# Kernel tuning notes

Hardware: AMD Instinct MI355X
Metric: run time of the kernel (lower is better)

## Reference

```python
import jax, jax.numpy as jnp
import numpy as np

B, R, C, E, H = 2, 16, 512, 1024, 16
D = E // H  # head_dim = 64


def setup_inputs() -> dict:
    key = jax.random.key(0)
    ks = jax.random.split(key, 9)
    s = 1.0 / np.sqrt(E)
    return {
        "x": jax.random.normal(ks[0], (B, R, C, E), dtype=jnp.float32),
        "wq": jax.random.uniform(ks[1], (E, E), jnp.float32, -s, s),
        "bq": jax.random.uniform(ks[2], (E,), jnp.float32, -s, s),
        "wk": jax.random.uniform(ks[3], (E, E), jnp.float32, -s, s),
        "bk": jax.random.uniform(ks[4], (E,), jnp.float32, -s, s),
        "wv": jax.random.uniform(ks[5], (E, E), jnp.float32, -s, s),
        "bv": jax.random.uniform(ks[6], (E,), jnp.float32, -s, s),
        "wo": jax.random.uniform(ks[7], (E, E), jnp.float32, -s, s),
        "bo": jax.random.uniform(ks[8], (E,), jnp.float32, -s, s),
    }


def reference(x, wq, bq, wk, bk, wv, bv, wo, bo):
    b, r, c, e = x.shape
    # projections: [b,r,c,e] -> [b,r,h,c,d]
    def split_heads(t):
        return t.reshape(b, r, c, H, D).transpose(0, 1, 3, 2, 4)
    q = split_heads(x @ wq + bq)
    k = split_heads(x @ wk + bk)
    v = split_heads(x @ wv + bv)
    scale = 1.0 / jnp.sqrt(jnp.asarray(D, x.dtype))
    logits = jnp.einsum('brhqd,brhkd->brhqk', q, k) * scale
    probs = jax.nn.softmax(logits, axis=-1)
    ctx = jnp.einsum('brhqk,brhkd->brhqd', probs, v)
    ctx = ctx.transpose(0, 1, 3, 2, 4).reshape(b, r, c, e)
    return ctx @ wo + bo
```

## Files before the change

kernel.cpp:

```cpp
#include <hip/hip_runtime.h>
#include <hip/hip_bf16.h>
#include <hip/hip_fp16.h>
#include <math.h>

typedef _Float16 half8 __attribute__((ext_vector_type(8)));
typedef __attribute__((ext_vector_type(4))) float floatx4;

constexpr int Bc = 2, Rc = 16, Cc = 512, Ec = 1024, Hc = 16, Dc = 64;
#define QSCALE 0.180336880111120425f

__device__ inline void gl_lds16(const void* g, void* l) {
  __builtin_amdgcn_global_load_lds(
      (const __attribute__((address_space(1))) void*)g,
      (__attribute__((address_space(3))) void*)l, 16, 0, 0);
}
__device__ inline unsigned short f2h(float f) {
  __half h = __float2half_rn(f);
  return *(unsigned short*)&h;
}
__device__ inline unsigned int pack_h2(float lo, float hi) {
  __half2 p = __float22half2_rn(make_float2(lo, hi));
  return *(unsigned int*)&p;
}

__global__ __launch_bounds__(256) void cvt_x(const float* __restrict__ x,
                                             unsigned short* __restrict__ xh) {
  const size_t base = ((size_t)blockIdx.x * 256 + threadIdx.x) * 8;
  float4 a = *(const float4*)(x + base);
  float4 b = *(const float4*)(x + base + 4);
  uint4 o;
  o.x = pack_h2(a.x, a.y);
  o.y = pack_h2(a.z, a.w);
  o.z = pack_h2(b.x, b.y);
  o.w = pack_h2(b.z, b.w);
  *(uint4*)(xh + base) = o;
}

__global__ __launch_bounds__(256) void wprep(
    const float* __restrict__ w0, const float* __restrict__ w1,
    const float* __restrict__ w2, const float* __restrict__ w3,
    unsigned short* __restrict__ t0, unsigned short* __restrict__ t1,
    unsigned short* __restrict__ t2, unsigned short* __restrict__ t3) {
  __shared__ float tile[64][65];
  const int z = blockIdx.z;
  const float* W = (z == 0) ? w0 : (z == 1) ? w1 : (z == 2) ? w2 : w3;
  unsigned short* T = (z == 0) ? t0 : (z == 1) ? t1 : (z == 2) ? t2 : t3;
  const int tid = threadIdx.x;
  const int bk = blockIdx.x * 64, bn = blockIdx.y * 64;
#pragma unroll
  for (int p = 0; p < 16; ++p) {
    int idx = p * 256 + tid;
    int lk = idx >> 6, lnn = idx & 63;
    tile[lnn][lk] = W[(size_t)(bk + lk) * 1024 + bn + lnn];
  }
  __syncthreads();
  const int lane = tid & 63, sub = tid >> 6;
  const int lr = lane & 15, quad = lane >> 4;
#pragma unroll
  for (int tl = 0; tl < 2; ++tl) {
    float v[8];
#pragma unroll
    for (int jj = 0; jj < 8; ++jj)
      v[jj] = tile[sub * 16 + lr][tl * 32 + quad * 8 + jj];
    uint4 o;
    o.x = pack_h2(v[0], v[1]);
    o.y = pack_h2(v[2], v[3]);
    o.z = pack_h2(v[4], v[5]);
    o.w = pack_h2(v[6], v[7]);
    const size_t n16 = (size_t)(bn >> 4) + sub;
    const size_t tt = (size_t)(bk >> 5) + tl;
    *(uint4*)(T + ((n16 * 32 + tt) * 64 + lane) * 8) = o;
  }
}

#define WAIT_VM(N)                                                            \
  {                                                                           \
    __builtin_amdgcn_sched_barrier(0);                                        \
    asm volatile("s_waitcnt vmcnt(" #N ")" ::: "memory");                     \
    __builtin_amdgcn_sched_barrier(0);                                        \
  }

#define STG_A(SBUF, KT)                                                       \
  {                                                                           \
    _Pragma("unroll") for (int l_ = 0; l_ < 2; ++l_) {                        \
      const int r0_ = l_ * 128 + w * 16;                                      \
      gl_lds16(Ab + (size_t)r0_ * 1024 + glan + (size_t)(KT) * 32,            \
               As + (SBUF) * 8192 + r0_ * 32);                                \
    }                                                                         \
  }

#define BLOAD(FB, KT)                                                         \
  _Pragma("unroll") for (int j_ = 0; j_ < 4; ++j_) FB[j_] =                   \
      *(const half8*)(Bf + bqoff + (size_t)j_ * 16384 + (size_t)(KT) * 512);

#define DSRA(NBUF, FA)                                                        \
  _Pragma("unroll") for (int i_ = 0; i_ < 8; ++i_) FA[i_] =                   \
      *(const half8*)&As[(NBUF) * 8192 + (wm + i_ * 16 + lr) * 32 + swq];

#define MFMA32(FA, FB)                                                        \
  _Pragma("unroll") for (int i_ = 0; i_ < 8; ++i_)                            \
      _Pragma("unroll") for (int j_ = 0; j_ < 4; ++j_) acc[i_][j_] =          \
          __builtin_amdgcn_mfma_f32_16x16x32_f16(FA[i_], FB[j_],              \
                                                 acc[i_][j_], 0, 0, 0);

#define TSTEP(NBUF, SBUF, KSTG, KBLD, FA, FB, NFA, NFB, STGE, BLDE, DSRE,     \
              VMN, BARE)                                                      \
  {                                                                           \
    if (STGE) STG_A(SBUF, KSTG);                                              \
    if (BLDE) BLOAD(NFB, KBLD);                                               \
    if (DSRE) DSRA(NBUF, NFA);                                                \
    WAIT_VM(VMN);                                                             \
    __builtin_amdgcn_s_setprio(1);                                            \
    MFMA32(FA, FB);                                                           \
    __builtin_amdgcn_s_setprio(0);                                            \
    if (BARE) {                                                               \
      __builtin_amdgcn_s_barrier();                                           \
      __builtin_amdgcn_sched_barrier(0);                                      \
    }                                                                         \
  }

template <int MODE>
__global__ __launch_bounds__(512, 2) void gemm256(
    const unsigned short* __restrict__ gA, const unsigned short* __restrict__ gB,
    const float* __restrict__ bq, const float* __restrict__ bk,
    const float* __restrict__ bv, unsigned short* __restrict__ qout,
    unsigned short* __restrict__ kout, unsigned short* __restrict__ vout,
    float* __restrict__ fout, const float* __restrict__ bo) {
  __shared__ unsigned short As[4 * 8192];
  const int tid = threadIdx.x;
  const int w = tid >> 6, ln = tid & 63;
  const int lr = ln & 15, quad = ln >> 4;
  const int wm = (w >> 2) * 128, wn = (w & 3) * 64;
  int bm, bn;
  if (MODE == 0) {
    const int swz = (blockIdx.x & 7) * 96 + (blockIdx.x >> 3);
    bm = (swz / 12) * 256;
    bn = (swz % 12) * 256;
  } else {
    const int swz = (blockIdx.x & 7) * 32 + (blockIdx.x >> 3);
    bm = (swz >> 2) * 256;
    bn = (swz & 3) * 256;
  }
  const unsigned short* Ab = gA + (size_t)bm * 1024;
  const unsigned short* Bf = gB;
  const size_t bqoff =
      (size_t)((bn >> 4) + (w & 3) * 4) * 16384 + (size_t)ln * 8;
  const int glan = (ln >> 2) * 1024 + (((ln & 3) ^ ((ln >> 3) & 3)) << 3);
  const int swq = ((quad ^ ((lr >> 1) & 3)) << 3);

  floatx4 acc[8][4];
#pragma unroll
  for (int i = 0; i < 8; ++i)
#pragma unroll
    for (int j = 0; j < 4; ++j) acc[i][j] = (floatx4)(0.f);
  half8 fa0[8], fa1[8], fb0[4], fb1[4];

  STG_A(0, 0);
  STG_A(1, 1);
  STG_A(2, 2);
  BLOAD(fb0, 0);
  WAIT_VM(6);
  __builtin_amdgcn_s_barrier();
  __builtin_amdgcn_sched_barrier(0);
  DSRA(0, fa0);

  for (int tt = 0; tt < 7; ++tt) {
    const int k4 = tt * 4;
    TSTEP(1, 3, k4 + 3, k4 + 1, fa0, fb0, fa1, fb1, 1, 1, 1, 6, 1);
    TSTEP(2, 0, k4 + 4, k4 + 2, fa1, fb1, fa0, fb0, 1, 1, 1, 6, 1);
    TSTEP(3, 1, k4 + 5, k4 + 3, fa0, fb0, fa1, fb1, 1, 1, 1, 6, 1);
    TSTEP(0, 2, k4 + 6, k4 + 4, fa1, fb1, fa0, fb0, 1, 1, 1, 6, 1);
  }
  TSTEP(1, 3, 31, 29, fa0, fb0, fa1, fb1, 1, 1, 1, 6, 1);
  TSTEP(2, 0, 0, 30, fa1, fb1, fa0, fb0, 0, 1, 1, 4, 1);
  TSTEP(3, 0, 0, 31, fa0, fb0, fa1, fb1, 0, 1, 1, 4, 1);
  TSTEP(0, 0, 0, 0, fa1, fb1, fa0, fb0, 0, 0, 0, 0, 0);

  const int q4 = quad * 4;
  const bool odd = ln & 1;
  if constexpr (MODE == 0) {
    const int z = bn >> 10;
    const float* bias = (z == 0) ? bq : (z == 1) ? bk : bv;
    const int czb = (bn & 1023) + wn;
#pragma unroll
    for (int i = 0; i < 8; ++i) {
#pragma unroll
      for (int j = 0; j < 4; ++j) {
        const int colz = czb + j * 16 + lr;
        float v[4];
#pragma unroll
        for (int r = 0; r < 4; ++r) v[r] = acc[i][j][r] + bias[colz];
        const int m0 = bm + wm + i * 16 + q4;
        const int h = colz >> 6, d = colz & 63;
        const int brr = m0 >> 9, c0 = m0 & 511;
        const size_t hb = ((size_t)brr * 16 + h) * 32768;
        if (z == 2) {
          uint2 o;
          o.x = pack_h2(v[0], v[1]);
          o.y = pack_h2(v[2], v[3]);
          *(uint2*)(vout + hb + (size_t)d * 512 + c0) = o;
        } else {
          unsigned short* outp = (z == 0) ? qout : kout;
          if (z == 0) {
#pragma unroll
            for (int r = 0; r < 4; ++r) v[r] *= QSCALE;
          }
#pragma unroll
          for (int rp = 0; rp < 2; ++rp) {
            float a = v[2 * rp], b = v[2 * rp + 1];
            float ax = __shfl_xor(a, 1), bx = __shfl_xor(b, 1);
            unsigned int u = odd ? pack_h2(bx, b) : pack_h2(a, ax);
            const int c = c0 + 2 * rp + (odd ? 1 : 0);
            const int dd = d & ~1;
            *(unsigned int*)(outp + hb + (size_t)c * 64 + dd) = u;
          }
        }
      }
    }
  } else {
#pragma unroll
    for (int i = 0; i < 8; ++i)
#pragma unroll
      for (int j = 0; j < 4; ++j) {
        const int col = bn + wn + j * 16 + lr;
#pragma unroll
        for (int r = 0; r < 4; ++r) {
          const int m = bm + wm + i * 16 + q4 + r;
          fout[(size_t)m * 1024 + col] = acc[i][j][r] + bo[col];
        }
      }
  }
}

__global__ __launch_bounds__(256, 4) void attn_mfma(
    const unsigned short* __restrict__ Qh, const unsigned short* __restrict__ Kb,
    const unsigned short* __restrict__ Vt, unsigned short* __restrict__ Ctx) {
  __shared__ unsigned short Ks[64 * 64];
  __shared__ unsigned short Vs[64 * 64];
  __shared__ unsigned short Ps[128][72];

  const int t = threadIdx.x;
  const int w = t >> 6, ln = t & 63;
  const int lane15 = ln & 15, quad = ln >> 4;
  const bool odd = ln & 1;
  const int bh = (blockIdx.x & 7) * 64 + (blockIdx.x >> 5);
  const int qb = ((blockIdx.x >> 3) & 3) * 128;

  half8 qf[2][2];
  {
    const size_t qbase =
        ((size_t)bh * 512 + qb + w * 32 + lane15) * 64 + quad * 8;
#pragma unroll
    for (int i = 0; i < 2; ++i)
#pragma unroll
      for (int c = 0; c < 2; ++c)
        qf[i][c] = *(const half8*)(Qh + qbase + (size_t)i * 16 * 64 + c * 32);
  }

  floatx4 oacc[2][4];
#pragma unroll
  for (int i = 0; i < 2; ++i)
#pragma unroll
    for (int dj = 0; dj < 4; ++dj) oacc[i][dj] = (floatx4)(0.f);
  float lsum[2][4];
#pragma unroll
  for (int i = 0; i < 2; ++i)
#pragma unroll
    for (int r = 0; r < 4; ++r) lsum[i][r] = 0.f;

  const unsigned short* kgb = Kb + (size_t)bh * 32768;
  const unsigned short* vgb = Vt + (size_t)bh * 32768;

  uint4 k0r, k1r, v0r, v1r;
#define LDK(P, KT)                                                            \
  (*(const uint4*)((const char*)kgb + (size_t)(KT) * 128 +                    \
                   (size_t)((P) * 256 + t) * 16))
#define LDV(P, KT)                                                            \
  (*(const uint4*)((const char*)vgb + (size_t)(KT) * 2 +                      \
                   (size_t)(((P) * 256 + t) >> 3) * 1024 +                    \
                   (((P) * 256 + t) & 7) * 16))
#define AT_LOAD(KT)                                                           \
  { k0r = LDK(0, KT); k1r = LDK(1, KT); v0r = LDV(0, KT); v1r = LDV(1, KT); }
#define STK(P, R)                                                             \
  {                                                                           \
    const int s_ = (P) * 256 + t, kr_ = s_ >> 3, kc_ = s_ & 7;                \
    *(uint4*)((char*)Ks + kr_ * 128 + ((kc_ ^ (kr_ & 7)) << 4)) = R;          \
  }
#define STV(P, R)                                                             \
  {                                                                           \
    const int s_ = (P) * 256 + t, vr_ = s_ >> 3, vc_ = s_ & 7;                \
    *(uint4*)((char*)Vs + vr_ * 128 + ((vc_ ^ (vr_ & 7)) << 4)) = R;          \
  }
#define AT_WRITE                                                              \
  { STK(0, k0r); STK(1, k1r); STV(0, v0r); STV(1, v1r); }

  AT_LOAD(0);
  AT_WRITE;

#pragma unroll
  for (int ktt = 0; ktt < 8; ++ktt) {
    __syncthreads();

    floatx4 sacc[2][4];
#pragma unroll
    for (int i = 0; i < 2; ++i)
#pragma unroll
      for (int j = 0; j < 4; ++j) sacc[i][j] = (floatx4)(0.f);
    __builtin_amdgcn_s_setprio(1);
#pragma unroll
    for (int j = 0; j < 4; ++j) {
      const int krow = j * 16 + lane15;
      const unsigned short* kr = Ks + krow * 64;
      half8 kf0 = *(const half8*)(kr + ((quad ^ (krow & 7)) << 3));
      half8 kf1 = *(const half8*)(kr + (((4 + quad) ^ (krow & 7)) << 3));
#pragma unroll
      for (int i = 0; i < 2; ++i) {
        sacc[i][j] = __builtin_amdgcn_mfma_f32_16x16x32_f16(qf[i][0], kf0,
                                                            sacc[i][j], 0, 0, 0);
        sacc[i][j] = __builtin_amdgcn_mfma_f32_16x16x32_f16(qf[i][1], kf1,
                                                            sacc[i][j], 0, 0, 0);
      }
    }
    __builtin_amdgcn_s_setprio(0);

#pragma unroll
    for (int i = 0; i < 2; ++i) {
#pragma unroll
      for (int rp = 0; rp < 2; ++rp) {
        const int rA = rp * 2, rB = rA + 1;
        const int row = w * 32 + i * 16 + quad * 4 + rA + (odd ? 1 : 0);
        unsigned short* prow = &Ps[row][lane15 & ~1];
#pragma unroll
        for (int j = 0; j < 4; ++j) {
          const float pA = exp2f(sacc[i][j][rA]);
          const float pB = exp2f(sacc[i][j][rB]);
          lsum[i][rA] += pA;
          lsum[i][rB] += pB;
          const float an = __shfl_xor(pA, 1);
          const float bn = __shfl_xor(pB, 1);
          const float lo = odd ? bn : pA;
          const float hi = odd ? pB : an;
          *(unsigned int*)(prow + j * 16) = pack_h2(lo, hi);
        }
      }
    }

    if (ktt < 7) {
      AT_LOAD((ktt + 1) * 64);
      __builtin_amdgcn_sched_barrier(0);
    }

    __builtin_amdgcn_s_setprio(1);
#pragma unroll
    for (int kc = 0; kc < 2; ++kc) {
      half8 pa0 = *(const half8*)&Ps[w * 32 + lane15][kc * 32 + quad * 8];
      half8 pa1 = *(const half8*)&Ps[w * 32 + 16 + lane15][kc * 32 + quad * 8];
#pragma unroll
      for (int dj = 0; dj < 4; ++dj) {
        const int drow = dj * 16 + lane15;
        half8 vf = *(const half8*)(
            Vs + drow * 64 + (((kc * 4 + quad) ^ (drow & 7)) << 3));
        oacc[0][dj] = __builtin_amdgcn_mfma_f32_16x16x32_f16(pa0, vf,
                                                             oacc[0][dj], 0, 0, 0);
        oacc[1][dj] = __builtin_amdgcn_mfma_f32_16x16x32_f16(pa1, vf,
                                                             oacc[1][dj], 0, 0, 0);
      }
    }
    __builtin_amdgcn_s_setprio(0);

    __syncthreads();
    if (ktt < 7) AT_WRITE;
  }

  float invl[2][4];
#pragma unroll
  for (int i = 0; i < 2; ++i)
#pragma unroll
    for (int r = 0; r < 4; ++r) {
      float ls = lsum[i][r];
#pragma unroll
      for (int off = 1; off < 16; off <<= 1) ls += __shfl_xor(ls, off);
      invl[i][r] = 1.f / ls;
    }
  const int br = bh >> 4, h = bh & 15;
  const size_t mbase = (size_t)br * 512 + qb + w * 32;
#pragma unroll
  for (int i = 0; i < 2; ++i)
#pragma unroll
    for (int dj = 0; dj < 4; ++dj) {
      const int e = h * 64 + dj * 16 + lane15;
      const int ee = e & ~1;
#pragma unroll
      for (int rp = 0; rp < 2; ++rp) {
        const int rA = 2 * rp, rB = rA + 1;
        float a = oacc[i][dj][rA] * invl[i][rA];
        float b = oacc[i][dj][rB] * invl[i][rB];
        float ax = __shfl_xor(a, 1), bx = __shfl_xor(b, 1);
        unsigned int u = odd ? pack_h2(bx, b) : pack_h2(a, ax);
        const size_t m = mbase + i * 16 + quad * 4 + rA + (odd ? 1 : 0);
        *(unsigned int*)(Ctx + m * 1024 + ee) = u;
      }
    }
}

extern "C" void kernel_launch(void* const* d_in, const int* in_sizes, int n_in,
                              void* d_out, int out_size, void* d_ws,
                              size_t ws_size, hipStream_t stream) {
  const float* x = (const float*)d_in[0];
  const float* wq = (const float*)d_in[1];
  const float* bq = (const float*)d_in[2];
  const float* wk = (const float*)d_in[3];
  const float* bk = (const float*)d_in[4];
  const float* wv = (const float*)d_in[5];
  const float* bv = (const float*)d_in[6];
  const float* wo = (const float*)d_in[7];
  const float* bo = (const float*)d_in[8];
  float* out = (float*)d_out;

  char* w = (char*)d_ws;
  const size_t MiB = 1ull << 20;
  unsigned short* qbuf = (unsigned short*)(w + 0 * MiB);
  unsigned short* kbuf = (unsigned short*)(w + 32 * MiB);
  unsigned short* vtb = (unsigned short*)(w + 64 * MiB);
  unsigned short* xh = (unsigned short*)(w + 96 * MiB);
  unsigned short* ctx = (unsigned short*)(w + 128 * MiB);
  unsigned short* wqh = (unsigned short*)(w + 160 * MiB);
  unsigned short* wkh = (unsigned short*)(w + 162 * MiB);
  unsigned short* wvh = (unsigned short*)(w + 164 * MiB);
  unsigned short* woh = (unsigned short*)(w + 166 * MiB);

  cvt_x<<<8192, 256, 0, stream>>>(x, xh);
  wprep<<<dim3(16, 16, 4), 256, 0, stream>>>(wq, wk, wv, wo, wqh, wkh, wvh,
                                             woh);

  gemm256<0><<<768, 512, 0, stream>>>(xh, wqh, bq, bk, bv, qbuf, kbuf, vtb,
                                      nullptr, nullptr);

  attn_mfma<<<2048, 256, 0, stream>>>(qbuf, kbuf, vtb, ctx);

  gemm256<1><<<256, 512, 0, stream>>>(ctx, woh, nullptr, nullptr, nullptr,
                                      nullptr, nullptr, nullptr, out, bo);
}
```

Before: 345.0 us.

## Double-buffer K/V via direct global-to-LDS loads and keep P in registers

The attention kernel now stages K and V tiles with global_load_lds straight into double-buffered LDS slots, prefetching the next tile while the current one is computed. This drops one of the two barriers per iteration. It also swaps the MFMA operand order so scores come out transposed, which lets P stay in registers and be reshuffled with ds_bpermute instead of round-tripping through an LDS P buffer. Row sums become per-lane column sums reduced with two shuffles, and output stores become 8-byte vector writes. The risks are the correctness of the swizzle and permutation indexing, plus the extra bpermute traffic.

```diff
diff --git a/kernel.cpp b/kernel.cpp
--- a/kernel.cpp
+++ b/kernel.cpp
@@ -235,14 +235,12 @@
 __global__ __launch_bounds__(256, 4) void attn_mfma(
     const unsigned short* __restrict__ Qh, const unsigned short* __restrict__ Kb,
     const unsigned short* __restrict__ Vt, unsigned short* __restrict__ Ctx) {
-  __shared__ unsigned short Ks[64 * 64];
-  __shared__ unsigned short Vs[64 * 64];
-  __shared__ unsigned short Ps[128][72];
+  __shared__ unsigned short Kd[2 * 4096];
+  __shared__ unsigned short Vd[2 * 4096];
 
   const int t = threadIdx.x;
   const int w = t >> 6, ln = t & 63;
   const int lane15 = ln & 15, quad = ln >> 4;
-  const bool odd = ln & 1;
   const int bh = (blockIdx.x & 7) * 64 + (blockIdx.x >> 5);
   const int qb = ((blockIdx.x >> 3) & 3) * 128;
 
@@ -257,49 +255,41 @@
         qf[i][c] = *(const half8*)(Qh + qbase + (size_t)i * 16 * 64 + c * 32);
   }
 
-  floatx4 oacc[2][4];
+  floatx4 oaccT[2][4];
 #pragma unroll
   for (int i = 0; i < 2; ++i)
 #pragma unroll
-    for (int dj = 0; dj < 4; ++dj) oacc[i][dj] = (floatx4)(0.f);
-  float lsum[2][4];
-#pragma unroll
-  for (int i = 0; i < 2; ++i)
-#pragma unroll
-    for (int r = 0; r < 4; ++r) lsum[i][r] = 0.f;
+    for (int dj = 0; dj < 4; ++dj) oaccT[i][dj] = (floatx4)(0.f);
+  float lsum[2] = {0.f, 0.f};
 
   const unsigned short* kgb = Kb + (size_t)bh * 32768;
   const unsigned short* vgb = Vt + (size_t)bh * 32768;
 
-  uint4 k0r, k1r, v0r, v1r;
-#define LDK(P, KT)                                                            \
-  (*(const uint4*)((const char*)kgb + (size_t)(KT) * 128 +                    \
-                   (size_t)((P) * 256 + t) * 16))
-#define LDV(P, KT)                                                            \
-  (*(const uint4*)((const char*)vgb + (size_t)(KT) * 2 +                      \
-                   (size_t)(((P) * 256 + t) >> 3) * 1024 +                    \
-                   (((P) * 256 + t) & 7) * 16))
-#define AT_LOAD(KT)                                                           \
-  { k0r = LDK(0, KT); k1r = LDK(1, KT); v0r = LDV(0, KT); v1r = LDV(1, KT); }
-#define STK(P, R)                                                             \
+  const int klo = (((ln & 7) ^ (ln >> 3)) << 3);
+  const int krow_l = w * 8 + (ln >> 3);
+  const int idxA = ((32 * ((ln >> 4) & 1)) + lane15) * 4;
+  const int idxB = idxA + 64;
+  const bool lowh = ln < 32;
+
+#define AT_STAGE(SLOT, KT)                                                    \
   {                                                                           \
-    const int s_ = (P) * 256 + t, kr_ = s_ >> 3, kc_ = s_ & 7;                \
-    *(uint4*)((char*)Ks + kr_ * 128 + ((kc_ ^ (kr_ & 7)) << 4)) = R;          \
-  }
-#define STV(P, R)                                                             \
-  {                                                                           \
-    const int s_ = (P) * 256 + t, vr_ = s_ >> 3, vc_ = s_ & 7;                \
-    *(uint4*)((char*)Vs + vr_ * 128 + ((vc_ ^ (vr_ & 7)) << 4)) = R;          \
-  }
-#define AT_WRITE                                                              \
-  { STK(0, k0r); STK(1, k1r); STV(0, v0r); STV(1, v1r); }
-
-  AT_LOAD(0);
-  AT_WRITE;
+    gl_lds16(kgb + (size_t)((KT) + krow_l) * 64 + klo,                        \
+             Kd + (SLOT) * 4096 + w * 512);                                   \
+    gl_lds16(kgb + (size_t)((KT) + 32 + krow_l) * 64 + klo,                   \
+             Kd + (SLOT) * 4096 + 2048 + w * 512);                            \
+    gl_lds16(vgb + (size_t)krow_l * 512 + (KT) + klo,                         \
+             Vd + (SLOT) * 4096 + w * 512);                                   \
+    gl_lds16(vgb + (size_t)(32 + krow_l) * 512 + (KT) + klo,                  \
+             Vd + (SLOT) * 4096 + 2048 + w * 512);                            \
+  }
+
+  AT_STAGE(0, 0);
+  __syncthreads();
 
 #pragma unroll
   for (int ktt = 0; ktt < 8; ++ktt) {
-    __syncthreads();
+    const int slot = ktt & 1;
+    if (ktt < 7) AT_STAGE(slot ^ 1, (ktt + 1) * 64);
 
     floatx4 sacc[2][4];
 #pragma unroll
@@ -310,97 +300,95 @@
 #pragma unroll
     for (int j = 0; j < 4; ++j) {
       const int krow = j * 16 + lane15;
-      const unsigned short* kr = Ks + krow * 64;
+      const unsigned short* kr = Kd + slot * 4096 + krow * 64;
       half8 kf0 = *(const half8*)(kr + ((quad ^ (krow & 7)) << 3));
       half8 kf1 = *(const half8*)(kr + (((4 + quad) ^ (krow & 7)) << 3));
 #pragma unroll
       for (int i = 0; i < 2; ++i) {
-        sacc[i][j] = __builtin_amdgcn_mfma_f32_16x16x32_f16(qf[i][0], kf0,
+        sacc[i][j] = __builtin_amdgcn_mfma_f32_16x16x32_f16(kf0, qf[i][0],
                                                             sacc[i][j], 0, 0, 0);
-        sacc[i][j] = __builtin_amdgcn_mfma_f32_16x16x32_f16(qf[i][1], kf1,
+        sacc[i][j] = __builtin_amdgcn_mfma_f32_16x16x32_f16(kf1, qf[i][1],
                                                             sacc[i][j], 0, 0, 0);
       }
     }
     __builtin_amdgcn_s_setprio(0);
 
-#pragma unroll
-    for (int i = 0; i < 2; ++i) {
-#pragma unroll
-      for (int rp = 0; rp < 2; ++rp) {
-        const int rA = rp * 2, rB = rA + 1;
-        const int row = w * 32 + i * 16 + quad * 4 + rA + (odd ? 1 : 0);
-        unsigned short* prow = &Ps[row][lane15 & ~1];
-#pragma unroll
-        for (int j = 0; j < 4; ++j) {
-          const float pA = exp2f(sacc[i][j][rA]);
-          const float pB = exp2f(sacc[i][j][rB]);
-          lsum[i][rA] += pA;
-          lsum[i][rB] += pB;
-          const float an = __shfl_xor(pA, 1);
-          const float bn = __shfl_xor(pB, 1);
-          const float lo = odd ? bn : pA;
-          const float hi = odd ? pB : an;
-          *(unsigned int*)(prow + j * 16) = pack_h2(lo, hi);
-        }
-      }
-    }
-
-    if (ktt < 7) {
-      AT_LOAD((ktt + 1) * 64);
-      __builtin_amdgcn_sched_barrier(0);
-    }
+    unsigned int pk[2][4][2];
+#pragma unroll
+    for (int i = 0; i < 2; ++i)
+#pragma unroll
+      for (int j = 0; j < 4; ++j) {
+        const float p0 = exp2f(sacc[i][j][0]);
+        const float p1 = exp2f(sacc[i][j][1]);
+        const float p2 = exp2f(sacc[i][j][2]);
+        const float p3 = exp2f(sacc[i][j][3]);
+        lsum[i] += (p0 + p1) + (p2 + p3);
+        pk[i][j][0] = pack_h2(p0, p1);
+        pk[i][j][1] = pack_h2(p2, p3);
+      }
 
     __builtin_amdgcn_s_setprio(1);
 #pragma unroll
     for (int kc = 0; kc < 2; ++kc) {
-      half8 pa0 = *(const half8*)&Ps[w * 32 + lane15][kc * 32 + quad * 8];
-      half8 pa1 = *(const half8*)&Ps[w * 32 + 16 + lane15][kc * 32 + quad * 8];
+      unsigned int bfr[2][4];
+#pragma unroll
+      for (int i = 0; i < 2; ++i) {
+        const int a0 = __builtin_amdgcn_ds_bpermute(idxA, (int)pk[i][2 * kc][0]);
+        const int c0 = __builtin_amdgcn_ds_bpermute(idxA, (int)pk[i][2 * kc + 1][0]);
+        const int a1 = __builtin_amdgcn_ds_bpermute(idxA, (int)pk[i][2 * kc][1]);
+        const int c1 = __builtin_amdgcn_ds_bpermute(idxA, (int)pk[i][2 * kc + 1][1]);
+        const int a2 = __builtin_amdgcn_ds_bpermute(idxB, (int)pk[i][2 * kc][0]);
+        const int c2 = __builtin_amdgcn_ds_bpermute(idxB, (int)pk[i][2 * kc + 1][0]);
+        const int a3 = __builtin_amdgcn_ds_bpermute(idxB, (int)pk[i][2 * kc][1]);
+        const int c3 = __builtin_amdgcn_ds_bpermute(idxB, (int)pk[i][2 * kc + 1][1]);
+        bfr[i][0] = (unsigned int)(lowh ? a0 : c0);
+        bfr[i][1] = (unsigned int)(lowh ? a1 : c1);
+        bfr[i][2] = (unsigned int)(lowh ? a2 : c2);
+        bfr[i][3] = (unsigned int)(lowh ? a3 : c3);
+      }
+      half8 pb0 = *(half8*)&bfr[0][0];
+      half8 pb1 = *(half8*)&bfr[1][0];
 #pragma unroll
       for (int dj = 0; dj < 4; ++dj) {
         const int drow = dj * 16 + lane15;
-        half8 vf = *(const half8*)(
-            Vs + drow * 64 + (((kc * 4 + quad) ^ (drow & 7)) << 3));
-        oacc[0][dj] = __builtin_amdgcn_mfma_f32_16x16x32_f16(pa0, vf,
-                                                             oacc[0][dj], 0, 0, 0);
-        oacc[1][dj] = __builtin_amdgcn_mfma_f32_16x16x32_f16(pa1, vf,
-                                                             oacc[1][dj], 0, 0, 0);
+        half8 vf = *(const half8*)(Vd + slot * 4096 + drow * 64 +
+                                   (((kc * 4 + quad) ^ (drow & 7)) << 3));
+        oaccT[0][dj] = __builtin_amdgcn_mfma_f32_16x16x32_f16(vf, pb0,
+                                                              oaccT[0][dj], 0, 0, 0);
+        oaccT[1][dj] = __builtin_amdgcn_mfma_f32_16x16x32_f16(vf, pb1,
+                                                              oaccT[1][dj], 0, 0, 0);
       }
     }
     __builtin_amdgcn_s_setprio(0);
 
-    __syncthreads();
-    if (ktt < 7) AT_WRITE;
-  }
-
-  float invl[2][4];
-#pragma unroll
-  for (int i = 0; i < 2; ++i)
-#pragma unroll
-    for (int r = 0; r < 4; ++r) {
-      float ls = lsum[i][r];
-#pragma unroll
-      for (int off = 1; off < 16; off <<= 1) ls += __shfl_xor(ls, off);
-      invl[i][r] = 1.f / ls;
-    }
+    if (ktt < 7) __syncthreads();
+  }
+
+  float invl[2];
+#pragma unroll
+  for (int i = 0; i < 2; ++i) {
+    float ls = lsum[i];
+    ls += __shfl_xor(ls, 16);
+    ls += __shfl_xor(ls, 32);
+    invl[i] = 1.f / ls;
+  }
   const int br = bh >> 4, h = bh & 15;
   const size_t mbase = (size_t)br * 512 + qb + w * 32;
 #pragma unroll
-  for (int i = 0; i < 2; ++i)
+  for (int i = 0; i < 2; ++i) {
+    const size_t m = mbase + i * 16 + lane15;
 #pragma unroll
     for (int dj = 0; dj < 4; ++dj) {
-      const int e = h * 64 + dj * 16 + lane15;
-      const int ee = e & ~1;
-#pragma unroll
-      for (int rp = 0; rp < 2; ++rp) {
-        const int rA = 2 * rp, rB = rA + 1;
-        float a = oacc[i][dj][rA] * invl[i][rA];
-        float b = oacc[i][dj][rB] * invl[i][rB];
-        float ax = __shfl_xor(a, 1), bx = __shfl_xor(b, 1);
-        unsigned int u = odd ? pack_h2(bx, b) : pack_h2(a, ax);
-        const size_t m = mbase + i * 16 + quad * 4 + rA + (odd ? 1 : 0);
-        *(unsigned int*)(Ctx + m * 1024 + ee) = u;
-      }
+      const float o0 = oaccT[i][dj][0] * invl[i];
+      const float o1 = oaccT[i][dj][1] * invl[i];
+      const float o2 = oaccT[i][dj][2] * invl[i];
+      const float o3 = oaccT[i][dj][3] * invl[i];
+      uint2 u;
+      u.x = pack_h2(o0, o1);
+      u.y = pack_h2(o2, o3);
+      *(uint2*)(Ctx + m * 1024 + h * 64 + dj * 16 + quad * 4) = u;
     }
+  }
 }
 
 extern "C" void kernel_launch(void* const* d_in, const int* in_sizes, int n_in,
```

Result: slower. 511.8 us (+48.3%).
